# Kernel tuning notes

Measured on AMD Instinct MI355X. Metric: run time of the kernel, lower is better.

Reference implementation:

```python
import jax, jax.numpy as jnp
import numpy as np

GAMMA = 0.99
GAE_LAMBDA = 0.95
DONE_PROB = 0.01  # sparse episode terminations, typical for long-horizon trading envs


def setup_inputs() -> dict:
    key = jax.random.key(0)
    k1, k2, k3 = jax.random.split(key, 3)
    T, N = 2048, 4096  # rollout_len, num_envs
    rewards = jax.random.normal(k1, (T, N), dtype=jnp.float32)
    values = jax.random.normal(k2, (T, N), dtype=jnp.float32)
    dones = (jax.random.uniform(k3, (T, N)) < DONE_PROB).astype(jnp.float32)
    return {"rewards": rewards, "values": values, "dones": dones}


def reference(rewards, values, dones):
    # rewards/values/dones: [T, N]
    T, N = rewards.shape
    # bootstrap: beyond the last step, next_value = 0 and next_done = 1
    next_value = jnp.concatenate([values[1:], jnp.zeros((1, N), values.dtype)], axis=0)
    next_done = jnp.concatenate([dones[1:], jnp.ones((1, N), dones.dtype)], axis=0)
    nonterminal = 1.0 - next_done                      # [T, N]
    delta = rewards + GAMMA * next_value * nonterminal - values  # [T, N]

    def step(last_adv, xs):
        d, nt = xs                                     # each [N]
        adv = d + GAMMA * GAE_LAMBDA * nt * last_adv
        return adv, adv

    init = jnp.zeros((N,), rewards.dtype)
    _, advantages = jax.lax.scan(step, init, (delta, nonterminal), reverse=True)
    returns = advantages + values
    return advantages, returns
```

## Files before the change

kernel.cpp:

```cpp
#include <hip/hip_runtime.h>


#define T_LEN    2048
#define N_ENV    4096
#define NV4      (N_ENV / 4)
#define N_CHUNKS 128
#define CHUNK_L  (T_LEN / N_CHUNKS)
#define NBLK     ((N_CHUNKS * NV4) / 256)

static constexpr float GAMMA = 0.99f;
static constexpr float GL    = 0.99f * 0.95f;

__global__ __launch_bounds__(256) void gae_sum(
    const float4* __restrict__ rewards,
    const float4* __restrict__ values,
    const float4* __restrict__ dones,
    float4* __restrict__ Aout,
    float4* __restrict__ Pout)
{
    const int idx = blockIdx.x * blockDim.x + threadIdx.x;
    const int n4 = idx & (NV4 - 1);
    const int c  = idx >> 10;
    const int t_hi = c * CHUNK_L + (CHUNK_L - 1);

    float4 v_next, d_next;
    if (c == N_CHUNKS - 1) {
        v_next = make_float4(0.f, 0.f, 0.f, 0.f);
        d_next = make_float4(1.f, 1.f, 1.f, 1.f);
    } else {
        v_next = values[(t_hi + 1) * NV4 + n4];
        d_next = dones [(t_hi + 1) * NV4 + n4];
    }

    float4 A = make_float4(1.f, 1.f, 1.f, 1.f);
    float4 P = make_float4(0.f, 0.f, 0.f, 0.f);

    #pragma unroll
    for (int i = 0; i < CHUNK_L; ++i) {
        const int t = t_hi - i;
        const float4 r = rewards[t * NV4 + n4];
        const float4 v = values [t * NV4 + n4];
        const float4 d = dones  [t * NV4 + n4];
        #define STEP(X) { \
            const float nt    = 1.0f - d_next.X; \
            const float delta = fmaf(GAMMA * v_next.X, nt, r.X) - v.X; \
            const float co    = GL * nt; \
            P.X = fmaf(co, P.X, delta); \
            A.X = co * A.X; \
            v_next.X = v.X; d_next.X = d.X; }
        STEP(x) STEP(y) STEP(z) STEP(w)
        #undef STEP
    }
    Aout[idx] = A;
    Pout[idx] = P;
}

__global__ __launch_bounds__(128) void gae_scan(
    const float4* __restrict__ Ain,
    const float4* __restrict__ Pin,
    float4* __restrict__ Inc)
{
    __shared__ float4 sA[2][N_CHUNKS];
    __shared__ float4 sP[2][N_CHUNKS];
    const int n4 = blockIdx.x;
    const int c  = threadIdx.x;

    float4 a = Ain[c * NV4 + n4];
    float4 p = Pin[c * NV4 + n4];
    int cur = 0;
    sA[0][c] = a; sP[0][c] = p;
    __syncthreads();

    #pragma unroll
    for (int d = 1; d < N_CHUNKS; d <<= 1) {
        float4 na = a, np = p;
        if (c + d < N_CHUNKS) {
            const float4 a2 = sA[cur][c + d];
            const float4 p2 = sP[cur][c + d];
            na.x = a.x * a2.x;  np.x = fmaf(a.x, p2.x, p.x);
            na.y = a.y * a2.y;  np.y = fmaf(a.y, p2.y, p.y);
            na.z = a.z * a2.z;  np.z = fmaf(a.z, p2.z, p.z);
            na.w = a.w * a2.w;  np.w = fmaf(a.w, p2.w, p.w);
        }
        sA[cur ^ 1][c] = na; sP[cur ^ 1][c] = np;
        __syncthreads();
        a = na; p = np; cur ^= 1;
    }

    float4 inc = (c == N_CHUNKS - 1) ? make_float4(0.f, 0.f, 0.f, 0.f)
                                     : sP[cur][c + 1];
    Inc[c * NV4 + n4] = inc;
}

__global__ __launch_bounds__(256) void gae_out(
    const float4* __restrict__ rewards,
    const float4* __restrict__ values,
    const float4* __restrict__ dones,
    const float4* __restrict__ Inc,
    float4* __restrict__ out)
{
    const int idx = blockIdx.x * blockDim.x + threadIdx.x;
    const int n4 = idx & (NV4 - 1);
    const int c  = idx >> 10;
    const int t_hi = c * CHUNK_L + (CHUNK_L - 1);

    float4 adv = Inc[idx];

    float4 v_next, d_next;
    if (c == N_CHUNKS - 1) {
        v_next = make_float4(0.f, 0.f, 0.f, 0.f);
        d_next = make_float4(1.f, 1.f, 1.f, 1.f);
    } else {
        v_next = values[(t_hi + 1) * NV4 + n4];
        d_next = dones [(t_hi + 1) * NV4 + n4];
    }

    #pragma unroll
    for (int i = 0; i < CHUNK_L; ++i) {
        const int t = t_hi - i;
        const float4 r = rewards[t * NV4 + n4];
        const float4 v = values [t * NV4 + n4];
        const float4 d = dones  [t * NV4 + n4];
        float4 ret;
        #define STEP(X) { \
            const float nt    = 1.0f - d_next.X; \
            const float delta = fmaf(GAMMA * v_next.X, nt, r.X) - v.X; \
            const float co    = GL * nt; \
            adv.X = fmaf(co, adv.X, delta); \
            ret.X = adv.X + v.X; \
            v_next.X = v.X; d_next.X = d.X; }
        STEP(x) STEP(y) STEP(z) STEP(w)
        #undef STEP
        out[t * NV4 + n4]           = adv;
        out[(T_LEN + t) * NV4 + n4] = ret;
    }
}

__global__ __launch_bounds__(256) void gae_phase23_fb(
    const float4* __restrict__ rewards,
    const float4* __restrict__ values,
    const float4* __restrict__ dones,
    const float4* __restrict__ Ain,
    const float4* __restrict__ Pin,
    float4* __restrict__ out)
{
    const int idx = blockIdx.x * blockDim.x + threadIdx.x;
    const int n4 = idx & (NV4 - 1);
    const int c  = idx >> 10;
    const int t_hi = c * CHUNK_L + (CHUNK_L - 1);

    float4 adv = make_float4(0.f, 0.f, 0.f, 0.f);
    #pragma unroll 4
    for (int c2 = N_CHUNKS - 1; c2 > c; --c2) {
        const float4 a = Ain[c2 * NV4 + n4];
        const float4 p = Pin[c2 * NV4 + n4];
        adv.x = fmaf(a.x, adv.x, p.x);
        adv.y = fmaf(a.y, adv.y, p.y);
        adv.z = fmaf(a.z, adv.z, p.z);
        adv.w = fmaf(a.w, adv.w, p.w);
    }
    float4 v_next, d_next;
    if (c == N_CHUNKS - 1) {
        v_next = make_float4(0.f, 0.f, 0.f, 0.f);
        d_next = make_float4(1.f, 1.f, 1.f, 1.f);
    } else {
        v_next = values[(t_hi + 1) * NV4 + n4];
        d_next = dones [(t_hi + 1) * NV4 + n4];
    }
    #pragma unroll
    for (int i = 0; i < CHUNK_L; ++i) {
        const int t = t_hi - i;
        const float4 r = rewards[t * NV4 + n4];
        const float4 v = values [t * NV4 + n4];
        const float4 d = dones  [t * NV4 + n4];
        float4 ret;
        #define STEP(X) { \
            const float nt    = 1.0f - d_next.X; \
            const float delta = fmaf(GAMMA * v_next.X, nt, r.X) - v.X; \
            const float co    = GL * nt; \
            adv.X = fmaf(co, adv.X, delta); \
            ret.X = adv.X + v.X; \
            v_next.X = v.X; d_next.X = d.X; }
        STEP(x) STEP(y) STEP(z) STEP(w)
        #undef STEP
        out[t * NV4 + n4]           = adv;
        out[(T_LEN + t) * NV4 + n4] = ret;
    }
}

extern "C" void kernel_launch(void* const* d_in, const int* in_sizes, int n_in,
                              void* d_out, int out_size, void* d_ws, size_t ws_size,
                              hipStream_t stream) {
    const float4* rewards = (const float4*)d_in[0];
    const float4* values  = (const float4*)d_in[1];
    const float4* dones   = (const float4*)d_in[2];
    float4* out = (float4*)d_out;

    const size_t entries = (size_t)N_CHUNKS * NV4;
    float4* A   = (float4*)d_ws;
    float4* P   = A + entries;
    float4* Inc = P + entries;

    if (ws_size >= 3 * entries * sizeof(float4)) {
        gae_sum <<<NBLK, 256, 0, stream>>>(rewards, values, dones, A, P);
        gae_scan<<<NV4,  128, 0, stream>>>(A, P, Inc);
        gae_out <<<NBLK, 256, 0, stream>>>(rewards, values, dones, Inc, out);
    } else {
        gae_sum      <<<NBLK, 256, 0, stream>>>(rewards, values, dones, A, P);
        gae_phase23_fb<<<NBLK, 256, 0, stream>>>(rewards, values, dones, A, P, out);
    }
}
```

Measured before the change: 168.0 us.

## Compress dones into a per-float4 bitmask and double the chunk count

The first pass now also writes a 4-bit termination mask per float4 of `dones`, one byte each, into workspace. The output pass reads this mask instead of the full float `dones` array, which cuts its read traffic by about a third. The chunk count is also doubled to 256, shortening each thread's serial run and raising parallelism, at the cost of larger A/P/Inc workspace arrays and a bigger scan. The fallback path still writes the mask even when the workspace is too small for it, which risks an out-of-bounds write.

```diff
diff --git a/kernel.cpp b/kernel.cpp
--- a/kernel.cpp
+++ b/kernel.cpp
@@ -4,7 +4,7 @@
 #define T_LEN    2048
 #define N_ENV    4096
 #define NV4      (N_ENV / 4)
-#define N_CHUNKS 128
+#define N_CHUNKS 256
 #define CHUNK_L  (T_LEN / N_CHUNKS)
 #define NBLK     ((N_CHUNKS * NV4) / 256)
 
@@ -16,7 +16,8 @@
     const float4* __restrict__ values,
     const float4* __restrict__ dones,
     float4* __restrict__ Aout,
-    float4* __restrict__ Pout)
+    float4* __restrict__ Pout,
+    unsigned char* __restrict__ mask)
 {
     const int idx = blockIdx.x * blockDim.x + threadIdx.x;
     const int n4 = idx & (NV4 - 1);
@@ -41,6 +42,10 @@
         const float4 r = rewards[t * NV4 + n4];
         const float4 v = values [t * NV4 + n4];
         const float4 d = dones  [t * NV4 + n4];
+        const unsigned char mb =
+            (unsigned char)((d.x != 0.f)      | ((d.y != 0.f) << 1) |
+                            ((d.z != 0.f) << 2) | ((d.w != 0.f) << 3));
+        mask[t * NV4 + n4] = mb;
         #define STEP(X) { \
             const float nt    = 1.0f - d_next.X; \
             const float delta = fmaf(GAMMA * v_next.X, nt, r.X) - v.X; \
@@ -55,7 +60,7 @@
     Pout[idx] = P;
 }
 
-__global__ __launch_bounds__(128) void gae_scan(
+__global__ __launch_bounds__(N_CHUNKS) void gae_scan(
     const float4* __restrict__ Ain,
     const float4* __restrict__ Pin,
     float4* __restrict__ Inc)
@@ -95,7 +100,7 @@
 __global__ __launch_bounds__(256) void gae_out(
     const float4* __restrict__ rewards,
     const float4* __restrict__ values,
-    const float4* __restrict__ dones,
+    const unsigned char* __restrict__ mask,
     const float4* __restrict__ Inc,
     float4* __restrict__ out)
 {
@@ -106,6 +111,61 @@
 
     float4 adv = Inc[idx];
 
+    float4 v_next;
+    unsigned int mb_next;
+    if (c == N_CHUNKS - 1) {
+        v_next  = make_float4(0.f, 0.f, 0.f, 0.f);
+        mb_next = 0xFu;
+    } else {
+        v_next  = values[(t_hi + 1) * NV4 + n4];
+        mb_next = mask  [(t_hi + 1) * NV4 + n4];
+    }
+
+    #pragma unroll
+    for (int i = 0; i < CHUNK_L; ++i) {
+        const int t = t_hi - i;
+        const float4 r = rewards[t * NV4 + n4];
+        const float4 v = values [t * NV4 + n4];
+        const unsigned int mb = mask[t * NV4 + n4];
+        float4 ret;
+        #define STEP(X, B) { \
+            const float nt    = (mb_next & (B)) ? 0.0f : 1.0f; \
+            const float delta = fmaf(GAMMA * v_next.X, nt, r.X) - v.X; \
+            const float co    = GL * nt; \
+            adv.X = fmaf(co, adv.X, delta); \
+            ret.X = adv.X + v.X; \
+            v_next.X = v.X; }
+        STEP(x, 1u) STEP(y, 2u) STEP(z, 4u) STEP(w, 8u)
+        #undef STEP
+        mb_next = mb;
+        out[t * NV4 + n4]           = adv;
+        out[(T_LEN + t) * NV4 + n4] = ret;
+    }
+}
+
+__global__ __launch_bounds__(256) void gae_phase23_fb(
+    const float4* __restrict__ rewards,
+    const float4* __restrict__ values,
+    const float4* __restrict__ dones,
+    const float4* __restrict__ Ain,
+    const float4* __restrict__ Pin,
+    float4* __restrict__ out)
+{
+    const int idx = blockIdx.x * blockDim.x + threadIdx.x;
+    const int n4 = idx & (NV4 - 1);
+    const int c  = idx >> 10;
+    const int t_hi = c * CHUNK_L + (CHUNK_L - 1);
+
+    float4 adv = make_float4(0.f, 0.f, 0.f, 0.f);
+    #pragma unroll 4
+    for (int c2 = N_CHUNKS - 1; c2 > c; --c2) {
+        const float4 a = Ain[c2 * NV4 + n4];
+        const float4 p = Pin[c2 * NV4 + n4];
+        adv.x = fmaf(a.x, adv.x, p.x);
+        adv.y = fmaf(a.y, adv.y, p.y);
+        adv.z = fmaf(a.z, adv.z, p.z);
+        adv.w = fmaf(a.w, adv.w, p.w);
+    }
     float4 v_next, d_next;
     if (c == N_CHUNKS - 1) {
         v_next = make_float4(0.f, 0.f, 0.f, 0.f);
@@ -114,7 +174,6 @@
         v_next = values[(t_hi + 1) * NV4 + n4];
         d_next = dones [(t_hi + 1) * NV4 + n4];
     }
-
     #pragma unroll
     for (int i = 0; i < CHUNK_L; ++i) {
         const int t = t_hi - i;
@@ -136,58 +195,6 @@
     }
 }
 
-__global__ __launch_bounds__(256) void gae_phase23_fb(
-    const float4* __restrict__ rewards,
-    const float4* __restrict__ values,
-    const float4* __restrict__ dones,
-    const float4* __restrict__ Ain,
-    const float4* __restrict__ Pin,
-    float4* __restrict__ out)
-{
-    const int idx = blockIdx.x * blockDim.x + threadIdx.x;
-    const int n4 = idx & (NV4 - 1);
-    const int c  = idx >> 10;
-    const int t_hi = c * CHUNK_L + (CHUNK_L - 1);
-
-    float4 adv = make_float4(0.f, 0.f, 0.f, 0.f);
-    #pragma unroll 4
-    for (int c2 = N_CHUNKS - 1; c2 > c; --c2) {
-        const float4 a = Ain[c2 * NV4 + n4];
-        const float4 p = Pin[c2 * NV4 + n4];
-        adv.x = fmaf(a.x, adv.x, p.x);
-        adv.y = fmaf(a.y, adv.y, p.y);
-        adv.z = fmaf(a.z, adv.z, p.z);
-        adv.w = fmaf(a.w, adv.w, p.w);
-    }
-    float4 v_next, d_next;
-    if (c == N_CHUNKS - 1) {
-        v_next = make_float4(0.f, 0.f, 0.f, 0.f);
-        d_next = make_float4(1.f, 1.f, 1.f, 1.f);
-    } else {
-        v_next = values[(t_hi + 1) * NV4 + n4];
-        d_next = dones [(t_hi + 1) * NV4 + n4];
-    }
-    #pragma unroll
-    for (int i = 0; i < CHUNK_L; ++i) {
-        const int t = t_hi - i;
-        const float4 r = rewards[t * NV4 + n4];
-        const float4 v = values [t * NV4 + n4];
-        const float4 d = dones  [t * NV4 + n4];
-        float4 ret;
-        #define STEP(X) { \
-            const float nt    = 1.0f - d_next.X; \
-            const float delta = fmaf(GAMMA * v_next.X, nt, r.X) - v.X; \
-            const float co    = GL * nt; \
-            adv.X = fmaf(co, adv.X, delta); \
-            ret.X = adv.X + v.X; \
-            v_next.X = v.X; d_next.X = d.X; }
-        STEP(x) STEP(y) STEP(z) STEP(w)
-        #undef STEP
-        out[t * NV4 + n4]           = adv;
-        out[(T_LEN + t) * NV4 + n4] = ret;
-    }
-}
-
 extern "C" void kernel_launch(void* const* d_in, const int* in_sizes, int n_in,
                               void* d_out, int out_size, void* d_ws, size_t ws_size,
                               hipStream_t stream) {
@@ -200,13 +207,16 @@
     float4* A   = (float4*)d_ws;
     float4* P   = A + entries;
     float4* Inc = P + entries;
-
-    if (ws_size >= 3 * entries * sizeof(float4)) {
-        gae_sum <<<NBLK, 256, 0, stream>>>(rewards, values, dones, A, P);
-        gae_scan<<<NV4,  128, 0, stream>>>(A, P, Inc);
-        gae_out <<<NBLK, 256, 0, stream>>>(rewards, values, dones, Inc, out);
-    } else {
-        gae_sum      <<<NBLK, 256, 0, stream>>>(rewards, values, dones, A, P);
+    unsigned char* mask = (unsigned char*)(Inc + entries);
+    const size_t needed = 3 * entries * sizeof(float4)
+                        + (size_t)T_LEN * NV4;
+
+    if (ws_size >= needed) {
+        gae_sum <<<NBLK, 256, 0, stream>>>(rewards, values, dones, A, P, mask);
+        gae_scan<<<NV4, N_CHUNKS, 0, stream>>>(A, P, Inc);
+        gae_out <<<NBLK, 256, 0, stream>>>(rewards, values, mask, Inc, out);
+    } else {
+        gae_sum      <<<NBLK, 256, 0, stream>>>(rewards, values, dones, A, P, mask);
         gae_phase23_fb<<<NBLK, 256, 0, stream>>>(rewards, values, dones, A, P, out);
     }
 }
```

Result: slower. 173.4 us (+3.2%).
